# Optimization experiments

Hardware: AMD Instinct MI355X
Metric: run time of the kernel (lower is better)

The kernel has to match this reference:

```python
import jax, jax.numpy as jnp
import numpy as np

N_SENT, B, S, D = 256, 512, 128, 1024
L, LATENT = 10331, 101  # int(sqrt(10331)) == 101


def setup_inputs() -> dict:
    key = jax.random.key(0)
    ks = jax.random.split(key, 16)
    inv = 1.0 / np.sqrt(D)
    return {
        'elmo_outputs': jax.random.normal(ks[0], (N_SENT, S, D), jnp.float32),
        'men_mask': jax.random.randint(ks[1], (B, S), 0, 2).astype(jnp.float32),
        'ctx_mask': jax.random.randint(ks[2], (B, S), 0, 2).astype(jnp.float32),
        'dist': jax.random.uniform(ks[3], (B, S), jnp.float32),
        'gathers': jax.random.randint(ks[4], (B,), 0, N_SENT),
        # nn.Linear weights, stored [out, in] as in torch
        'W_men_m': jax.random.normal(ks[5], (D, D), jnp.float32) * inv,
        'W_men_o': jax.random.normal(ks[6], (1, D), jnp.float32) * inv,
        'W_ctx_c': jax.random.normal(ks[7], (D, D), jnp.float32) * inv,
        'W_ctx_m': jax.random.normal(ks[8], (D, D), jnp.float32) * inv,
        'w_ctx_d': jax.random.normal(ks[9], (D,), jnp.float32),  # Linear(1, D) weight [D,1] squeezed
        'W_ctx_o': jax.random.normal(ks[10], (1, D), jnp.float32) * inv,
        'W_out': jax.random.normal(ks[11], (L, 2 * D), jnp.float32) * (1.0 / np.sqrt(2 * D)),
        'W_f2l': jax.random.normal(ks[12], (LATENT, 2 * D), jnp.float32) * (1.0 / np.sqrt(2 * D)),
        'W_l2l': jax.random.normal(ks[13], (L, LATENT), jnp.float32) * (1.0 / np.sqrt(LATENT)),
        'latent_scalar': jnp.array(0.1, jnp.float32),
    }


def reference(elmo_outputs, men_mask, ctx_mask, dist, gathers,
              W_men_m, W_men_o, W_ctx_c, W_ctx_m, w_ctx_d, W_ctx_o,
              W_out, W_f2l, W_l2l, latent_scalar):
    NEG = -10000.0
    # gather: sentence reps -> mention rows, [B, S, D]
    x = elmo_outputs[gathers]
    # mention additive attention
    men_h = jnp.tanh(jnp.einsum('bsd,ed->bse', x, W_men_m))
    men_score = jnp.einsum('bse,oe->bso', men_h, W_men_o)  # [B,S,1]
    men_score = men_score + (1.0 - men_mask[:, :, None]) * NEG
    men_attn = jax.nn.softmax(men_score, axis=1)
    men_repr = jnp.sum(x * men_attn, axis=1)  # [B, D]
    # context additive attention (dropout layers are identity in eval)
    ctx_h = jnp.tanh(
        jnp.einsum('bsd,ed->bse', x, W_ctx_c)
        + jnp.einsum('bd,ed->be', men_repr, W_ctx_m)[:, None, :]
        + dist[:, :, None] * w_ctx_d
    )
    ctx_score = jnp.einsum('bse,oe->bso', ctx_h, W_ctx_o)
    ctx_score = ctx_score + (1.0 - ctx_mask[:, :, None]) * NEG
    ctx_attn = jax.nn.softmax(ctx_score, axis=1)
    ctx_repr = jnp.sum(x * ctx_attn, axis=1)  # [B, D]
    final_repr = jnp.concatenate([men_repr, ctx_repr], axis=1)  # [B, 2D]
    outputs = final_repr @ W_out.T  # [B, L]
    latent_label = final_repr @ W_f2l.T  # [B, latent]
    outputs_latent = latent_label @ W_l2l.T  # [B, L]
    outputs = outputs + latent_scalar * outputs_latent
    return outputs, outputs_latent
```

## Files before the change

### kernel.cpp

```cpp
#include <hip/hip_runtime.h>
#include <hip/hip_bf16.h>

typedef __bf16 bf16x8 __attribute__((ext_vector_type(8)));
typedef float f32x4 __attribute__((ext_vector_type(4)));
typedef unsigned short u16x8 __attribute__((ext_vector_type(8)));

#define DEV __device__ __forceinline__

static constexpr int N_SENTC = 256, BB = 512, SS = 128, DD = 1024;
static constexpr int LL = 10331, LATENT = 101;
static constexpr int LPAD = 10368;
static constexpr int LATPAD = 128;

DEV float bf2f(unsigned short u) {
  unsigned v = (unsigned)u << 16;
  return __builtin_bit_cast(float, v);
}
DEV unsigned short f2bf(float f) {
  unsigned u = __builtin_bit_cast(unsigned, f);
  unsigned lsb = (u >> 16) & 1u;
  u += 0x7fffu + lsb;
  return (unsigned short)(u >> 16);
}

DEV float fast_tanh(float x) {
  float e = __expf(2.0f * x);
  return 1.0f - 2.0f / (e + 1.0f);
}

DEV void stage8(unsigned short* dst, const float* src) {
  float4 a = *(const float4*)src;
  float4 b = *(const float4*)(src + 4);
  unsigned short t[8];
  t[0] = f2bf(a.x); t[1] = f2bf(a.y); t[2] = f2bf(a.z); t[3] = f2bf(a.w);
  t[4] = f2bf(b.x); t[5] = f2bf(b.y); t[6] = f2bf(b.z); t[7] = f2bf(b.w);
  *(uint4*)dst = *(uint4*)t;
}

DEV void gl_lds16(const unsigned short* g, unsigned short* l) {
  __builtin_amdgcn_global_load_lds(
      (const __attribute__((address_space(1))) unsigned int*)g,
      (__attribute__((address_space(3))) unsigned int*)l, 16, 0, 0);
}

__global__ __launch_bounds__(256) void k_cvt(
    const float* __restrict__ src, unsigned short* __restrict__ dst, int n4) {
  for (int i = blockIdx.x * 256 + threadIdx.x; i < n4; i += gridDim.x * 256) {
    float4 v = ((const float4*)src)[i];
    unsigned short t[4] = {f2bf(v.x), f2bf(v.y), f2bf(v.z), f2bf(v.w)};
    ((uint2*)dst)[i] = *(const uint2*)t;
  }
}

__global__ __launch_bounds__(256) void k_cvt_pad(
    const float* __restrict__ src, unsigned short* __restrict__ dst,
    int srcR, int srcC, int dstC, int total) {
  for (int i = blockIdx.x * 256 + threadIdx.x; i < total; i += gridDim.x * 256) {
    int r = i / dstC, c = i - r * dstC;
    dst[i] = (r < srcR && c < srcC) ? f2bf(src[(size_t)r * srcC + c]) : (unsigned short)0;
  }
}

__global__ __launch_bounds__(512) void k_mc_gemm8(
    const unsigned short* __restrict__ Xb, const unsigned short* __restrict__ Wmb,
    const unsigned short* __restrict__ Wcb, const float* __restrict__ wo,
    float* __restrict__ score, unsigned short* __restrict__ Hc) {
  __shared__ __align__(16) unsigned short lds[2][2][2][8192];
  const int p = blockIdx.x;
  const int tid = threadIdx.x, w = tid >> 6, lane = tid & 63;
  const int lm = lane & 15, lq = lane >> 4;
  const int wr = w >> 2, wc = w & 3;
  const int stRow = w * 16 + (lane >> 2);
  const int stCol = ((lane & 3) * 8) ^ ((lane >> 5) << 4);
  const int rdCol = (lq * 16) ^ ((lane & 8) ? 32 : 0);
  const int aoff = (wr * 16 + lm) * 64 + rdCol;
  const int boff = (wc * 16 + lm) * 64 + rdCol;

  const unsigned short* aSrc;
  const unsigned short* bSrc;
  int rowBase, bcolBase;
  bool isMen;
  auto setTile = [&](int t) {
    const int vbid = p + 256 * t;
    const int lbid = (vbid & 7) * 128 + (vbid >> 3);
    const int colTile = lbid & 7, rowTile = lbid >> 3;
    rowBase = rowTile * 256;
    isMen = colTile < 4;
    bcolBase = (colTile & 3) * 256;
    aSrc = Xb + (size_t)(rowBase + stRow) * 1024 + stCol;
    bSrc = (isMen ? Wmb : Wcb) + (size_t)(bcolBase + stRow) * 1024 + stCol;
  };

  auto ST = [&](int op, int h, int kt, int buf) {
    const unsigned short* s = (op ? bSrc : aSrc) + (size_t)h * 131072 + kt * 64;
    unsigned short* d = &lds[buf][op][h][w * 512];
    gl_lds16(s, d);
    gl_lds16(s + 32, d + 4096);
  };
  auto PRO = [&]() {
    ST(0, 0, 0, 0); ST(1, 0, 0, 0); ST(0, 1, 0, 0); ST(1, 1, 0, 0);
    ST(0, 0, 1, 1); ST(1, 0, 1, 1); ST(0, 1, 1, 1);
  };

  setTile(0);
  PRO();

  for (int t = 0; t < 4; ++t) {
    asm volatile("s_waitcnt vmcnt(6)" ::: "memory");
    __builtin_amdgcn_s_barrier();

    f32x4 acc[8][4] = {};
    bf16x8 af0[4][2], af1[4][2], bfr[4][2];
    for (int kt = 0; kt < 16; ++kt) {
      const int buf = kt & 1;
      const char* A0 = (const char*)&lds[buf][0][0][0];
      const char* A1 = (const char*)&lds[buf][0][1][0];
      const char* B0 = (const char*)&lds[buf][1][0][0];
      const char* B1 = (const char*)&lds[buf][1][1][0];
#pragma unroll
      for (int m = 0; m < 4; ++m)
#pragma unroll
        for (int ks = 0; ks < 2; ++ks)
          af0[m][ks] = *(const bf16x8*)(A0 + aoff + m * 2048 + ks * 8192);
#pragma unroll
      for (int n = 0; n < 2; ++n)
#pragma unroll
        for (int ks = 0; ks < 2; ++ks)
          bfr[n][ks] = *(const bf16x8*)(B0 + boff + n * 4096 + ks * 8192);
      if (kt + 1 < 16) ST(1, 1, kt + 1, buf ^ 1);
      __builtin_amdgcn_s_barrier();
      __builtin_amdgcn_s_setprio(1);
#pragma unroll
      for (int m = 0; m < 4; ++m)
#pragma unroll
        for (int n = 0; n < 2; ++n)
#pragma unroll
          for (int ks = 0; ks < 2; ++ks)
            acc[m][n] = __builtin_amdgcn_mfma_f32_16x16x32_bf16(af0[m][ks], bfr[n][ks], acc[m][n], 0, 0, 0);
      __builtin_amdgcn_s_setprio(0);
      __builtin_amdgcn_s_barrier();
#pragma unroll
      for (int n = 0; n < 2; ++n)
#pragma unroll
        for (int ks = 0; ks < 2; ++ks)
          bfr[2 + n][ks] = *(const bf16x8*)(B1 + boff + n * 4096 + ks * 8192);
      if (kt + 2 < 16) ST(0, 0, kt + 2, buf);
      __builtin_amdgcn_s_barrier();
      __builtin_amdgcn_s_setprio(1);
#pragma unroll
      for (int m = 0; m < 4; ++m)
#pragma unroll
        for (int n = 0; n < 2; ++n)
#pragma unroll
          for (int ks = 0; ks < 2; ++ks)
            acc[m][2 + n] = __builtin_amdgcn_mfma_f32_16x16x32_bf16(af0[m][ks], bfr[2 + n][ks], acc[m][2 + n], 0, 0, 0);
      __builtin_amdgcn_s_setprio(0);
      __builtin_amdgcn_s_barrier();
#pragma unroll
      for (int m = 0; m < 4; ++m)
#pragma unroll
        for (int ks = 0; ks < 2; ++ks)
          af1[m][ks] = *(const bf16x8*)(A1 + aoff + m * 2048 + ks * 8192);
      if (kt + 2 < 16) ST(1, 0, kt + 2, buf);
      __builtin_amdgcn_s_barrier();
      __builtin_amdgcn_s_setprio(1);
#pragma unroll
      for (int m = 0; m < 4; ++m)
#pragma unroll
        for (int n = 0; n < 2; ++n)
#pragma unroll
          for (int ks = 0; ks < 2; ++ks)
            acc[4 + m][n] = __builtin_amdgcn_mfma_f32_16x16x32_bf16(af1[m][ks], bfr[n][ks], acc[4 + m][n], 0, 0, 0);
      __builtin_amdgcn_s_setprio(0);
      __builtin_amdgcn_s_barrier();
      if (kt + 2 < 16) ST(0, 1, kt + 2, buf);
      __builtin_amdgcn_s_barrier();
      __builtin_amdgcn_s_setprio(1);
#pragma unroll
      for (int m = 0; m < 4; ++m)
#pragma unroll
        for (int n = 0; n < 2; ++n)
#pragma unroll
          for (int ks = 0; ks < 2; ++ks)
            acc[4 + m][2 + n] = __builtin_amdgcn_mfma_f32_16x16x32_bf16(af1[m][ks], bfr[2 + n][ks], acc[4 + m][2 + n], 0, 0, 0);
      __builtin_amdgcn_s_setprio(0);
      if (kt < 14) {
        asm volatile("s_waitcnt vmcnt(6)" ::: "memory");
      } else {
        asm volatile("s_waitcnt vmcnt(0)" ::: "memory");
      }
      __builtin_amdgcn_s_barrier();
    }

    if (isMen) {
      float wov[4];
#pragma unroll
      for (int n = 0; n < 4; ++n) wov[n] = wo[bcolBase + n * 64 + wc * 16 + lm];
      float rsum[8][4];
#pragma unroll
      for (int m = 0; m < 8; ++m)
#pragma unroll
        for (int r = 0; r < 4; ++r) {
          float s = 0.f;
#pragma unroll
          for (int n = 0; n < 4; ++n) s += fast_tanh(acc[m][n][r]) * wov[n];
          rsum[m][r] = s;
        }
#pragma unroll
      for (int msk = 1; msk <= 8; msk <<= 1)
#pragma unroll
        for (int m = 0; m < 8; ++m)
#pragma unroll
          for (int r = 0; r < 4; ++r) rsum[m][r] += __shfl_xor(rsum[m][r], msk, 64);
      if (lm == 0) {
#pragma unroll
        for (int m = 0; m < 8; ++m)
#pragma unroll
          for (int r = 0; r < 4; ++r)
            atomicAdd(&score[rowBase + m * 32 + wr * 16 + lq * 4 + r], rsum[m][r]);
      }
    } else {
      const int cb0 = bcolBase + wc * 16 + lm;
#pragma unroll
      for (int m = 0; m < 8; ++m) {
        const int row = rowBase + m * 32 + wr * 16 + lq * 4;
#pragma unroll
        for (int n = 0; n < 4; ++n) {
          const int col = cb0 + n * 64;
#pragma unroll
          for (int r = 0; r < 4; ++r)
            Hc[(size_t)(row + r) * 1024 + col] = f2bf(acc[m][n][r]);
        }
      }
    }
    if (t < 3) {
      setTile(t + 1);
      PRO();
    }
  }
}

__global__ __launch_bounds__(256) void k_ctx_score(
    const unsigned short* __restrict__ Hc, const int* __restrict__ gathers,
    const float* __restrict__ cb, const float* __restrict__ wd,
    const float* __restrict__ wo, const float* __restrict__ dist,
    float* __restrict__ score) {
  const int b = blockIdx.x, tid = threadIdx.x, wave = tid >> 6, lane = tid & 63;
  const int n = gathers[b];
  __shared__ float cbl[1024], wdl[1024], wol[1024];
  for (int i = tid; i < 1024; i += 256) {
    cbl[i] = cb[b * 1024 + i];
    wdl[i] = wd[i];
    wol[i] = wo[i];
  }
  __syncthreads();
  for (int s = wave; s < 128; s += 4) {
    float d = dist[b * 128 + s];
    const unsigned short* hrow = &Hc[(size_t)(n * 128 + s) * 1024 + lane * 16];
    unsigned short hs[16];
    *(uint4*)hs = *(const uint4*)hrow;
    *(uint4*)(hs + 8) = *(const uint4*)(hrow + 8);
    float p = 0.f;
#pragma unroll
    for (int j = 0; j < 16; ++j) {
      int e = lane * 16 + j;
      p += fast_tanh(bf2f(hs[j]) + cbl[e] + d * wdl[e]) * wol[e];
    }
#pragma unroll
    for (int msk = 1; msk <= 32; msk <<= 1) p += __shfl_xor(p, msk, 64);
    if (lane == 0) score[b * 128 + s] = p;
  }
}

__global__ __launch_bounds__(256) void k_softb(
    const float* __restrict__ score_src, const float* __restrict__ mask,
    const unsigned short* __restrict__ Xb, const int* __restrict__ gathers,
    unsigned short* __restrict__ finalrb, int isCtx) {
  const int b = blockIdx.x, tid = threadIdx.x;
  const int n = gathers[b];
  __shared__ float attn[128];
  __shared__ float red[128 * 8];
  __shared__ float smax, ssum;
  if (tid < 128) {
    int srow = isCtx ? b : n;
    attn[tid] = score_src[srow * 128 + tid] + (1.0f - mask[b * 128 + tid]) * (-10000.0f);
  }
  __syncthreads();
  if (tid < 64) {
    float m = fmaxf(attn[tid], attn[tid + 64]);
#pragma unroll
    for (int msk = 1; msk <= 32; msk <<= 1) m = fmaxf(m, __shfl_xor(m, msk, 64));
    if (tid == 0) smax = m;
  }
  __syncthreads();
  if (tid < 128) attn[tid] = __expf(attn[tid] - smax);
  __syncthreads();
  if (tid < 64) {
    float s = attn[tid] + attn[tid + 64];
#pragma unroll
    for (int msk = 1; msk <= 32; msk <<= 1) s += __shfl_xor(s, msk, 64);
    if (tid == 0) ssum = 1.0f / s;
  }
  __syncthreads();
  if (tid < 128) attn[tid] *= ssum;
  __syncthreads();
  const unsigned short* xb = Xb + (size_t)n * 128 * 1024;
  const int c = tid & 127, h = tid >> 7;
  float acc[8] = {};
  for (int s = h; s < 128; s += 2) {
    float w = attn[s];
    u16x8 v = *(const u16x8*)&xb[(size_t)s * 1024 + c * 8];
#pragma unroll
    for (int j = 0; j < 8; ++j) acc[j] += w * bf2f(v[j]);
  }
  if (h == 1) {
#pragma unroll
    for (int j = 0; j < 8; ++j) red[c * 8 + j] = acc[j];
  }
  __syncthreads();
  if (h == 0) {
    unsigned short o[8];
#pragma unroll
    for (int j = 0; j < 8; ++j) o[j] = f2bf(acc[j] + red[c * 8 + j]);
    *(uint4*)&finalrb[(size_t)b * 2048 + (isCtx ? 1024 : 0) + c * 8] = *(uint4*)o;
  }
}

__global__ __launch_bounds__(256) void k_cb_gemm_b(
    const unsigned short* __restrict__ finalrb, const unsigned short* __restrict__ Wcmb,
    float* __restrict__ cb) {
  __shared__ __align__(16) unsigned short As[64 * 32];
  __shared__ __align__(16) unsigned short Bs[64 * 32];
  const int bid = blockIdx.x;
  const int rowBase = (bid >> 4) * 64, colBase = (bid & 15) * 64;
  const int tid = threadIdx.x, wave = tid >> 6, lane = tid & 63;
  const int lm = lane & 15, lq = lane >> 4;
  const int sr = tid >> 2, sc = (tid & 3) * 8;
  f32x4 acc[4] = {};
  for (int k0 = 0; k0 < 1024; k0 += 32) {
    __syncthreads();
    *(uint4*)&As[sr * 32 + sc] = *(const uint4*)&finalrb[(size_t)(rowBase + sr) * 2048 + k0 + sc];
    *(uint4*)&Bs[sr * 32 + sc] = *(const uint4*)&Wcmb[(size_t)(colBase + sr) * 1024 + k0 + sc];
    __syncthreads();
    bf16x8 af = *(const bf16x8*)&As[(wave * 16 + lm) * 32 + lq * 8];
#pragma unroll
    for (int j = 0; j < 4; ++j) {
      bf16x8 bfr = *(const bf16x8*)&Bs[(j * 16 + lm) * 32 + lq * 8];
      acc[j] = __builtin_amdgcn_mfma_f32_16x16x32_bf16(af, bfr, acc[j], 0, 0, 0);
    }
  }
#pragma unroll
  for (int j = 0; j < 4; ++j) {
    int col = colBase + j * 16 + lm;
#pragma unroll
    for (int r = 0; r < 4; ++r) {
      int row = rowBase + wave * 16 + lq * 4 + r;
      cb[row * 1024 + col] = acc[j][r];
    }
  }
}

__global__ __launch_bounds__(256) void k_lat_split(
    const unsigned short* __restrict__ finalrb, const unsigned short* __restrict__ Wf2lb,
    float* __restrict__ latf) {
  __shared__ __align__(16) unsigned short As[64 * 32];
  __shared__ __align__(16) unsigned short Bs[64 * 32];
  const int bid = blockIdx.x;
  const int ks = bid & 7;
  const int rowBase = ((bid >> 3) & 7) * 64;
  const int colBase = (bid >> 6) * 64;
  const int tid = threadIdx.x, wave = tid >> 6, lane = tid & 63;
  const int lm = lane & 15, lq = lane >> 4;
  const int sr = tid >> 2, sc = (tid & 3) * 8;
  f32x4 acc[4] = {};
  const int kEnd = ks * 256 + 256;
  for (int k0 = ks * 256; k0 < kEnd; k0 += 32) {
    __syncthreads();
    *(uint4*)&As[sr * 32 + sc] = *(const uint4*)&finalrb[(size_t)(rowBase + sr) * 2048 + k0 + sc];
    *(uint4*)&Bs[sr * 32 + sc] = *(const uint4*)&Wf2lb[(size_t)(colBase + sr) * 2048 + k0 + sc];
    __syncthreads();
    bf16x8 af = *(const bf16x8*)&As[(wave * 16 + lm) * 32 + lq * 8];
#pragma unroll
    for (int j = 0; j < 4; ++j) {
      bf16x8 bfr = *(const bf16x8*)&Bs[(j * 16 + lm) * 32 + lq * 8];
      acc[j] = __builtin_amdgcn_mfma_f32_16x16x32_bf16(af, bfr, acc[j], 0, 0, 0);
    }
  }
#pragma unroll
  for (int j = 0; j < 4; ++j) {
    int col = colBase + j * 16 + lm;
#pragma unroll
    for (int r = 0; r < 4; ++r) {
      int row = rowBase + wave * 16 + lq * 4 + r;
      atomicAdd(&latf[row * LATPAD + col], acc[j][r]);
    }
  }
}

__global__ __launch_bounds__(256) void k_out_gemm_f(
    const unsigned short* __restrict__ finalrb, const float* __restrict__ Wout,
    const unsigned short* __restrict__ latb, const unsigned short* __restrict__ Wl2lb,
    const float* __restrict__ lscale, float* __restrict__ out,
    float* __restrict__ outLat) {
  __shared__ __align__(16) unsigned short As[2 * 128 * 32];
  __shared__ __align__(16) unsigned short Bs[2 * 128 * 32];
  const int bid = blockIdx.x;
  const int xcd = bid & 7, idx = bid >> 3;
  const int rowTile = idx & 3, colTile = xcd + 8 * (idx >> 2);
  if (colTile >= 81) return;
  const int colBase = colTile * 128;
  const int rowBase = rowTile * 128;
  const int tid = threadIdx.x, wave = tid >> 6, lane = tid & 63;
  const int lm = lane & 15, lq = lane >> 4;
  const int wr = (wave & 1) * 64, wc = (wave >> 1) * 64;
  const int srow = wave * 32 + (lane >> 2);
  const int scol = (lane & 3) * 8;
  const float scal = lscale[0];
  const unsigned short* aPtr = finalrb + (size_t)(rowBase + srow) * 2048 + scol;
  const int br = tid >> 1, bh = tid & 1;
  const int bRow = colBase + br;
  const bool bv = bRow < LL;
  const float* bsrc = Wout + (size_t)bRow * 2048 + bh * 32;
  unsigned short* bdst = &Bs[bh * 4096 + br * 32];
  f32x4 acc[4][4] = {};
  for (int k0 = 0; k0 < 2048; k0 += 64) {
    __syncthreads();
    gl_lds16(aPtr + k0, As + wave * 1024);
    gl_lds16(aPtr + k0 + 16 * 2048, As + wave * 1024 + 512);
    gl_lds16(aPtr + k0 + 32, As + 4096 + wave * 1024);
    gl_lds16(aPtr + k0 + 32 + 16 * 2048, As + 4096 + wave * 1024 + 512);
    if (bv) {
      stage8(bdst, bsrc + k0);
      stage8(bdst + 8, bsrc + k0 + 8);
      stage8(bdst + 16, bsrc + k0 + 16);
      stage8(bdst + 24, bsrc + k0 + 24);
    } else {
      uint4 z = {0, 0, 0, 0};
      *(uint4*)bdst = z;
      *(uint4*)(bdst + 8) = z;
      *(uint4*)(bdst + 16) = z;
      *(uint4*)(bdst + 24) = z;
    }
    __syncthreads();
#pragma unroll
    for (int h = 0; h < 2; ++h) {
      bf16x8 af[4], bfr[4];
#pragma unroll
      for (int m = 0; m < 4; ++m)
        af[m] = *(const bf16x8*)&As[h * 4096 + (wr + m * 16 + lm) * 32 + lq * 8];
#pragma unroll
      for (int n = 0; n < 4; ++n)
        bfr[n] = *(const bf16x8*)&Bs[h * 4096 + (wc + n * 16 + lm) * 32 + lq * 8];
#pragma unroll
      for (int m = 0; m < 4; ++m)
#pragma unroll
        for (int n = 0; n < 4; ++n)
          acc[m][n] = __builtin_amdgcn_mfma_f32_16x16x32_bf16(af[m], bfr[n], acc[m][n], 0, 0, 0);
    }
  }
  const unsigned short* aPtr2 = latb + (size_t)(rowBase + srow) * LATPAD + scol;
  const unsigned short* bPtr2 = Wl2lb + (size_t)(colBase + srow) * LATPAD + scol;
  f32x4 acc2[4][4] = {};
  for (int k0 = 0; k0 < 128; k0 += 64) {
    __syncthreads();
#pragma unroll
    for (int h = 0; h < 2; ++h) {
      gl_lds16(aPtr2 + k0 + h * 32, As + h * 4096 + wave * 1024);
      gl_lds16(aPtr2 + k0 + h * 32 + 16 * LATPAD, As + h * 4096 + wave * 1024 + 512);
      gl_lds16(bPtr2 + k0 + h * 32, Bs + h * 4096 + wave * 1024);
      gl_lds16(bPtr2 + k0 + h * 32 + 16 * LATPAD, Bs + h * 4096 + wave * 1024 + 512);
    }
    __syncthreads();
#pragma unroll
    for (int h = 0; h < 2; ++h) {
      bf16x8 af[4], bfr[4];
#pragma unroll
      for (int m = 0; m < 4; ++m)
        af[m] = *(const bf16x8*)&As[h * 4096 + (wr + m * 16 + lm) * 32 + lq * 8];
#pragma unroll
      for (int n = 0; n < 4; ++n)
        bfr[n] = *(const bf16x8*)&Bs[h * 4096 + (wc + n * 16 + lm) * 32 + lq * 8];
#pragma unroll
      for (int m = 0; m < 4; ++m)
#pragma unroll
        for (int n = 0; n < 4; ++n)
          acc2[m][n] = __builtin_amdgcn_mfma_f32_16x16x32_bf16(af[m], bfr[n], acc2[m][n], 0, 0, 0);
    }
  }
#pragma unroll
  for (int m = 0; m < 4; ++m)
#pragma unroll
    for (int n = 0; n < 4; ++n) {
      int col = colBase + wc + n * 16 + lm;
      if (col < LL) {
#pragma unroll
        for (int r = 0; r < 4; ++r) {
          int row = rowBase + wr + m * 16 + lq * 4 + r;
          float lv = acc2[m][n][r];
          out[(size_t)row * LL + col] = acc[m][n][r] + scal * lv;
          outLat[(size_t)row * LL + col] = lv;
        }
      }
    }
}

__global__ __launch_bounds__(256) void k_men_gemm(
    const float* __restrict__ X, const float* __restrict__ Wm,
    const float* __restrict__ wo, float* __restrict__ score) {
  __shared__ __align__(16) unsigned short As[64 * 32];
  __shared__ __align__(16) unsigned short Bs[64 * 32];
  const int bid = blockIdx.x;
  const int rowBase = (bid >> 4) * 64, colBase = (bid & 15) * 64;
  const int tid = threadIdx.x, wave = tid >> 6, lane = tid & 63;
  const int lm = lane & 15, lq = lane >> 4;
  const int sr = tid >> 2, sc = (tid & 3) * 8;
  f32x4 acc[4] = {};
  for (int k0 = 0; k0 < 1024; k0 += 32) {
    __syncthreads();
    stage8(&As[sr * 32 + sc], &X[(size_t)(rowBase + sr) * 1024 + k0 + sc]);
    stage8(&Bs[sr * 32 + sc], &Wm[(size_t)(colBase + sr) * 1024 + k0 + sc]);
    __syncthreads();
    bf16x8 af = *(const bf16x8*)&As[(wave * 16 + lm) * 32 + lq * 8];
#pragma unroll
    for (int j = 0; j < 4; ++j) {
      bf16x8 bfr = *(const bf16x8*)&Bs[(j * 16 + lm) * 32 + lq * 8];
      acc[j] = __builtin_amdgcn_mfma_f32_16x16x32_bf16(af, bfr, acc[j], 0, 0, 0);
    }
  }
  float rsum[4] = {0.f, 0.f, 0.f, 0.f};
#pragma unroll
  for (int j = 0; j < 4; ++j) {
    float w = wo[colBase + j * 16 + lm];
#pragma unroll
    for (int r = 0; r < 4; ++r) rsum[r] += tanhf(acc[j][r]) * w;
  }
#pragma unroll
  for (int m = 1; m <= 8; m <<= 1)
#pragma unroll
    for (int r = 0; r < 4; ++r) rsum[r] += __shfl_xor(rsum[r], m, 64);
  if (lm == 0) {
    int row0 = rowBase + wave * 16 + lq * 4;
#pragma unroll
    for (int r = 0; r < 4; ++r) atomicAdd(&score[row0 + r], rsum[r]);
  }
}

__global__ __launch_bounds__(256) void k_ctx_gemm(
    const float* __restrict__ X, const int* __restrict__ gathers,
    const float* __restrict__ Wc, const float* __restrict__ wd,
    const float* __restrict__ wo, const float* __restrict__ dist,
    const float* __restrict__ cb, float* __restrict__ score) {
  __shared__ __align__(16) unsigned short As[64 * 32];
  __shared__ __align__(16) unsigned short Bs[64 * 32];
  const int bid = blockIdx.x;
  const int rowBase = (bid >> 4) * 64, colBase = (bid & 15) * 64;
  const int tid = threadIdx.x, wave = tid >> 6, lane = tid & 63;
  const int lm = lane & 15, lq = lane >> 4;
  const int sr = tid >> 2, sc = (tid & 3) * 8;
  const int row_g = rowBase + sr;
  const int srcRow = (gathers[row_g >> 7] << 7) + (row_g & 127);
  f32x4 acc[4] = {};
  for (int k0 = 0; k0 < 1024; k0 += 32) {
    __syncthreads();
    stage8(&As[sr * 32 + sc], &X[(size_t)srcRow * 1024 + k0 + sc]);
    stage8(&Bs[sr * 32 + sc], &Wc[(size_t)(colBase + sr) * 1024 + k0 + sc]);
    __syncthreads();
    bf16x8 af = *(const bf16x8*)&As[(wave * 16 + lm) * 32 + lq * 8];
#pragma unroll
    for (int j = 0; j < 4; ++j) {
      bf16x8 bfr = *(const bf16x8*)&Bs[(j * 16 + lm) * 32 + lq * 8];
      acc[j] = __builtin_amdgcn_mfma_f32_16x16x32_bf16(af, bfr, acc[j], 0, 0, 0);
    }
  }
  float rsum[4] = {0.f, 0.f, 0.f, 0.f};
#pragma unroll
  for (int j = 0; j < 4; ++j) {
    int col = colBase + j * 16 + lm;
    float w = wo[col];
    float wdv = wd[col];
#pragma unroll
    for (int r = 0; r < 4; ++r) {
      int rg = rowBase + wave * 16 + lq * 4 + r;
      int b = rg >> 7, s = rg & 127;
      float v = acc[j][r] + cb[b * 1024 + col] + dist[b * 128 + s] * wdv;
      rsum[r] += tanhf(v) * w;
    }
  }
#pragma unroll
  for (int m = 1; m <= 8; m <<= 1)
#pragma unroll
    for (int r = 0; r < 4; ++r) rsum[r] += __shfl_xor(rsum[r], m, 64);
  if (lm == 0) {
    int row0 = rowBase + wave * 16 + lq * 4;
#pragma unroll
    for (int r = 0; r < 4; ++r) atomicAdd(&score[row0 + r], rsum[r]);
  }
}

__global__ __launch_bounds__(256) void k_soft(
    const float* __restrict__ score_src, const float* __restrict__ mask,
    const float* __restrict__ X, const int* __restrict__ gathers,
    float* __restrict__ finalr, int isCtx) {
  const int b = blockIdx.x, tid = threadIdx.x;
  const int n = gathers[b];
  __shared__ float attn[128];
  __shared__ float smax, ssum;
  if (tid < 128) {
    int srow = isCtx ? b : n;
    attn[tid] = score_src[srow * 128 + tid] + (1.0f - mask[b * 128 + tid]) * (-10000.0f);
  }
  __syncthreads();
  if (tid == 0) {
    float m = attn[0];
    for (int i = 1; i < 128; ++i) m = fmaxf(m, attn[i]);
    smax = m;
  }
  __syncthreads();
  if (tid < 128) attn[tid] = expf(attn[tid] - smax);
  __syncthreads();
  if (tid == 0) {
    float s = 0.f;
    for (int i = 0; i < 128; ++i) s += attn[i];
    ssum = 1.0f / s;
  }
  __syncthreads();
  if (tid < 128) attn[tid] *= ssum;
  __syncthreads();
  const float* xb = &X[(size_t)(n << 7) * 1024];
  const int off = isCtx ? 1024 : 0;
  for (int d = tid; d < 1024; d += 256) {
    float a = 0.f;
#pragma unroll 8
    for (int s = 0; s < 128; ++s) a += attn[s] * xb[s * 1024 + d];
    finalr[b * 2048 + off + d] = a;
  }
}

__global__ __launch_bounds__(256) void k_cb_gemm(
    const float* __restrict__ finalr, const float* __restrict__ Wcm,
    float* __restrict__ cb) {
  __shared__ __align__(16) unsigned short As[64 * 32];
  __shared__ __align__(16) unsigned short Bs[64 * 32];
  const int bid = blockIdx.x;
  const int rowBase = (bid >> 4) * 64, colBase = (bid & 15) * 64;
  const int tid = threadIdx.x, wave = tid >> 6, lane = tid & 63;
  const int lm = lane & 15, lq = lane >> 4;
  const int sr = tid >> 2, sc = (tid & 3) * 8;
  f32x4 acc[4] = {};
  for (int k0 = 0; k0 < 1024; k0 += 32) {
    __syncthreads();
    stage8(&As[sr * 32 + sc], &finalr[(size_t)(rowBase + sr) * 2048 + k0 + sc]);
    stage8(&Bs[sr * 32 + sc], &Wcm[(size_t)(colBase + sr) * 1024 + k0 + sc]);
    __syncthreads();
    bf16x8 af = *(const bf16x8*)&As[(wave * 16 + lm) * 32 + lq * 8];
#pragma unroll
    for (int j = 0; j < 4; ++j) {
      bf16x8 bfr = *(const bf16x8*)&Bs[(j * 16 + lm) * 32 + lq * 8];
      acc[j] = __builtin_amdgcn_mfma_f32_16x16x32_bf16(af, bfr, acc[j], 0, 0, 0);
    }
  }
#pragma unroll
  for (int j = 0; j < 4; ++j) {
    int col = colBase + j * 16 + lm;
#pragma unroll
    for (int r = 0; r < 4; ++r) {
      int row = rowBase + wave * 16 + lq * 4 + r;
      cb[row * 1024 + col] = acc[j][r];
    }
  }
}

__global__ __launch_bounds__(256) void k_lat_gemm(
    const float* __restrict__ finalr, const float* __restrict__ Wf2l,
    float* __restrict__ lat) {
  __shared__ __align__(16) unsigned short As[64 * 32];
  __shared__ __align__(16) unsigned short Bs[64 * 32];
  const int rowBase = blockIdx.y * 64, colBase = blockIdx.x * 64;
  const int tid = threadIdx.x, wave = tid >> 6, lane = tid & 63;
  const int lm = lane & 15, lq = lane >> 4;
  const int sr = tid >> 2, sc = (tid & 3) * 8;
  f32x4 acc[4] = {};
  for (int k0 = 0; k0 < 2048; k0 += 32) {
    __syncthreads();
    stage8(&As[sr * 32 + sc], &finalr[(size_t)(rowBase + sr) * 2048 + k0 + sc]);
    int l = colBase + sr;
    if (l < LATENT) {
      stage8(&Bs[sr * 32 + sc], &Wf2l[(size_t)l * 2048 + k0 + sc]);
    } else {
      uint4 z = {0, 0, 0, 0};
      *(uint4*)&Bs[sr * 32 + sc] = z;
    }
    __syncthreads();
    bf16x8 af = *(const bf16x8*)&As[(wave * 16 + lm) * 32 + lq * 8];
#pragma unroll
    for (int j = 0; j < 4; ++j) {
      bf16x8 bfr = *(const bf16x8*)&Bs[(j * 16 + lm) * 32 + lq * 8];
      acc[j] = __builtin_amdgcn_mfma_f32_16x16x32_bf16(af, bfr, acc[j], 0, 0, 0);
    }
  }
#pragma unroll
  for (int j = 0; j < 4; ++j) {
    int col = colBase + j * 16 + lm;
    if (col < LATENT) {
#pragma unroll
      for (int r = 0; r < 4; ++r) {
        int row = rowBase + wave * 16 + lq * 4 + r;
        lat[row * LATENT + col] = acc[j][r];
      }
    }
  }
}

__global__ __launch_bounds__(256) void k_out_gemm(
    const float* __restrict__ finalr, const float* __restrict__ Wout,
    const float* __restrict__ lat, const float* __restrict__ Wl2l,
    const float* __restrict__ lscale, float* __restrict__ out,
    float* __restrict__ outLat) {
  __shared__ __align__(16) unsigned short As[64 * 32];
  __shared__ __align__(16) unsigned short Bs[64 * 32];
  const int rowBase = blockIdx.y * 64, colBase = blockIdx.x * 64;
  const int tid = threadIdx.x, wave = tid >> 6, lane = tid & 63;
  const int lm = lane & 15, lq = lane >> 4;
  const int sr = tid >> 2, sc = (tid & 3) * 8;
  const float scal = lscale[0];
  const int lrow = colBase + sr;
  const bool lvalid = (lrow < LL);
  f32x4 acc[4] = {};
  for (int k0 = 0; k0 < 2048; k0 += 32) {
    __syncthreads();
    stage8(&As[sr * 32 + sc], &finalr[(size_t)(rowBase + sr) * 2048 + k0 + sc]);
    if (lvalid) {
      stage8(&Bs[sr * 32 + sc], &Wout[(size_t)lrow * 2048 + k0 + sc]);
    } else {
      uint4 z = {0, 0, 0, 0};
      *(uint4*)&Bs[sr * 32 + sc] = z;
    }
    __syncthreads();
    bf16x8 af = *(const bf16x8*)&As[(wave * 16 + lm) * 32 + lq * 8];
#pragma unroll
    for (int j = 0; j < 4; ++j) {
      bf16x8 bfr = *(const bf16x8*)&Bs[(j * 16 + lm) * 32 + lq * 8];
      acc[j] = __builtin_amdgcn_mfma_f32_16x16x32_bf16(af, bfr, acc[j], 0, 0, 0);
    }
  }
  f32x4 acc2[4] = {};
  for (int k2 = 0; k2 < 128; k2 += 32) {
    __syncthreads();
    const int brow = rowBase + sr;
#pragma unroll
    for (int jj = 0; jj < 8; ++jj) {
      int idx = k2 + sc + jj;
      As[sr * 32 + sc + jj] = (idx < LATENT) ? f2bf(lat[brow * LATENT + idx]) : (unsigned short)0;
      Bs[sr * 32 + sc + jj] = (lvalid && idx < LATENT) ? f2bf(Wl2l[lrow * LATENT + idx]) : (unsigned short)0;
    }
    __syncthreads();
    bf16x8 af = *(const bf16x8*)&As[(wave * 16 + lm) * 32 + lq * 8];
#pragma unroll
    for (int j = 0; j < 4; ++j) {
      bf16x8 bfr = *(const bf16x8*)&Bs[(j * 16 + lm) * 32 + lq * 8];
      acc2[j] = __builtin_amdgcn_mfma_f32_16x16x32_bf16(af, bfr, acc2[j], 0, 0, 0);
    }
  }
#pragma unroll
  for (int j = 0; j < 4; ++j) {
    int col = colBase + j * 16 + lm;
    if (col < LL) {
#pragma unroll
      for (int r = 0; r < 4; ++r) {
        int row = rowBase + wave * 16 + lq * 4 + r;
        float lv = acc2[j][r];
        out[(size_t)row * LL + col] = acc[j][r] + scal * lv;
        outLat[(size_t)row * LL + col] = lv;
      }
    }
  }
}

extern "C" void kernel_launch(void* const* d_in, const int* in_sizes, int n_in,
                              void* d_out, int out_size, void* d_ws, size_t ws_size,
                              hipStream_t stream) {
  const float* X = (const float*)d_in[0];
  const float* men_mask = (const float*)d_in[1];
  const float* ctx_mask = (const float*)d_in[2];
  const float* dist = (const float*)d_in[3];
  const int* gathers = (const int*)d_in[4];
  const float* W_men_m = (const float*)d_in[5];
  const float* W_men_o = (const float*)d_in[6];
  const float* W_ctx_c = (const float*)d_in[7];
  const float* W_ctx_m = (const float*)d_in[8];
  const float* w_ctx_d = (const float*)d_in[9];
  const float* W_ctx_o = (const float*)d_in[10];
  const float* W_out = (const float*)d_in[11];
  const float* W_f2l = (const float*)d_in[12];
  const float* W_l2l = (const float*)d_in[13];
  const float* lscale = (const float*)d_in[14];
  float* out = (float*)d_out;
  float* outLat = out + (size_t)BB * LL;

  size_t off = 0;
  auto carve = [&](size_t bytes) {
    void* p = (char*)d_ws + off;
    off = (off + bytes + 255) & ~(size_t)255;
    return p;
  };
  float* sent_score = (float*)carve(32768 * 4);
  float* ctx_score = (float*)carve(65536 * 4);
  float* finalr = (float*)carve((size_t)512 * 2048 * 4);
  float* cb = (float*)carve((size_t)512 * 1024 * 4);
  float* lat = (float*)carve((size_t)512 * LATENT * 4);
  unsigned short* Xb = (unsigned short*)carve((size_t)32768 * 1024 * 2);
  unsigned short* Wmb = (unsigned short*)carve((size_t)1024 * 1024 * 2);
  unsigned short* Wcb = (unsigned short*)carve((size_t)1024 * 1024 * 2);
  unsigned short* Wcmb = (unsigned short*)carve((size_t)1024 * 1024 * 2);
  unsigned short* Hc = (unsigned short*)carve((size_t)32768 * 1024 * 2);
  unsigned short* Wf2lb = (unsigned short*)carve((size_t)LATPAD * 2048 * 2);
  unsigned short* Wl2lb = (unsigned short*)carve((size_t)LPAD * LATPAD * 2);
  unsigned short* finalrb = (unsigned short*)carve((size_t)512 * 2048 * 2);
  unsigned short* latb = (unsigned short*)carve((size_t)512 * LATPAD * 2);
  float* latf = (float*)carve((size_t)512 * LATPAD * 4);
  const bool fits = off <= ws_size;

  if (fits) {
    hipMemsetAsync(sent_score, 0, 32768 * sizeof(float), stream);
    hipMemsetAsync(latf, 0, (size_t)512 * LATPAD * sizeof(float), stream);
    k_cvt<<<8192, 256, 0, stream>>>(X, Xb, 32768 * 1024 / 4);
    k_cvt<<<1024, 256, 0, stream>>>(W_men_m, Wmb, 1024 * 1024 / 4);
    k_cvt<<<1024, 256, 0, stream>>>(W_ctx_c, Wcb, 1024 * 1024 / 4);
    k_cvt<<<1024, 256, 0, stream>>>(W_ctx_m, Wcmb, 1024 * 1024 / 4);
    k_cvt_pad<<<512, 256, 0, stream>>>(W_f2l, Wf2lb, LATENT, 2048, 2048, LATPAD * 2048);
    k_cvt_pad<<<1024, 256, 0, stream>>>(W_l2l, Wl2lb, LL, LATENT, LATPAD, LPAD * LATPAD);
    k_mc_gemm8<<<256, 512, 0, stream>>>(Xb, Wmb, Wcb, W_men_o, sent_score, Hc);
    k_softb<<<512, 256, 0, stream>>>(sent_score, men_mask, Xb, gathers, finalrb, 0);
    k_cb_gemm_b<<<128, 256, 0, stream>>>(finalrb, Wcmb, cb);
    k_ctx_score<<<512, 256, 0, stream>>>(Hc, gathers, cb, w_ctx_d, W_ctx_o, dist, ctx_score);
    k_softb<<<512, 256, 0, stream>>>(ctx_score, ctx_mask, Xb, gathers, finalrb, 1);
    k_lat_split<<<128, 256, 0, stream>>>(finalrb, Wf2lb, latf);
    k_cvt<<<64, 256, 0, stream>>>(latf, latb, 512 * LATPAD / 4);
    k_out_gemm_f<<<352, 256, 0, stream>>>(finalrb, W_out, latb, Wl2lb,
                                          lscale, out, outLat);
  } else {
    hipMemsetAsync(d_ws, 0, (32768 + 65536) * sizeof(float), stream);
    k_men_gemm<<<8192, 256, 0, stream>>>(X, W_men_m, W_men_o, sent_score);
    k_soft<<<512, 256, 0, stream>>>(sent_score, men_mask, X, gathers, finalr, 0);
    k_cb_gemm<<<128, 256, 0, stream>>>(finalr, W_ctx_m, cb);
    k_ctx_gemm<<<16384, 256, 0, stream>>>(X, gathers, W_ctx_c, w_ctx_d, W_ctx_o, dist, cb, ctx_score);
    k_soft<<<512, 256, 0, stream>>>(ctx_score, ctx_mask, X, gathers, finalr, 1);
    k_lat_gemm<<<dim3(2, 8), 256, 0, stream>>>(finalr, W_f2l, lat);
    k_out_gemm<<<dim3(162, 8), 256, 0, stream>>>(finalr, W_out, lat, W_l2l, lscale, out, outLat);
  }
}
```

Before: 657.4 us.

## Fuse weight conversions, fuse ctx score with softmax, prefetch W_out in out GEMM

Five weight-conversion launches are merged into one k_cvt_all kernel. The context score kernel now also does the masked softmax and the weighted sum over X, so the separate k_softb launch and the score round-trip through global memory go away. The output GEMM register-prefetches the next fp32 W_out slice before the barrier and uses manual waitcnt/s_barrier, so global loads overlap with MFMA work. This reduces launch overhead and hides load latency, at the cost of more registers and hand-managed synchronisation.

```diff
diff --git a/kernel.cpp b/kernel.cpp
--- a/kernel.cpp
+++ b/kernel.cpp
@@ -52,12 +52,47 @@
   }
 }
 
-__global__ __launch_bounds__(256) void k_cvt_pad(
-    const float* __restrict__ src, unsigned short* __restrict__ dst,
-    int srcR, int srcC, int dstC, int total) {
-  for (int i = blockIdx.x * 256 + threadIdx.x; i < total; i += gridDim.x * 256) {
-    int r = i / dstC, c = i - r * dstC;
-    dst[i] = (r < srcR && c < srcC) ? f2bf(src[(size_t)r * srcC + c]) : (unsigned short)0;
+__global__ __launch_bounds__(256) void k_cvt_all(
+    const float* __restrict__ Wm, const float* __restrict__ Wc,
+    const float* __restrict__ Wcm, const float* __restrict__ Wf2l,
+    const float* __restrict__ Wl2l,
+    unsigned short* __restrict__ Wmb, unsigned short* __restrict__ Wcb,
+    unsigned short* __restrict__ Wcmb, unsigned short* __restrict__ Wf2lb,
+    unsigned short* __restrict__ Wl2lb) {
+  const int NA = 3 * 262144;
+  const int NB = 65536;
+  const int NC = 331776;
+  for (int u = blockIdx.x * 256 + threadIdx.x; u < NA + NB + NC; u += gridDim.x * 256) {
+    if (u < NA) {
+      int which = u >> 18, off = u & 262143;
+      const float* s = which == 0 ? Wm : (which == 1 ? Wc : Wcm);
+      unsigned short* d = which == 0 ? Wmb : (which == 1 ? Wcb : Wcmb);
+      float4 v = ((const float4*)s)[off];
+      unsigned short t[4] = {f2bf(v.x), f2bf(v.y), f2bf(v.z), f2bf(v.w)};
+      ((uint2*)d)[off] = *(const uint2*)t;
+    } else if (u < NA + NB) {
+      int off = u - NA;
+      int r = off >> 9;
+      if (r < LATENT) {
+        float4 v = ((const float4*)Wf2l)[off];
+        unsigned short t[4] = {f2bf(v.x), f2bf(v.y), f2bf(v.z), f2bf(v.w)};
+        ((uint2*)Wf2lb)[off] = *(const uint2*)t;
+      } else {
+        ((uint2*)Wf2lb)[off] = make_uint2(0, 0);
+      }
+    } else {
+      int off = u - NA - NB;
+      int idx = off * 4;
+      int r = idx >> 7, c0 = idx & 127;
+      unsigned short t[4];
+#pragma unroll
+      for (int j = 0; j < 4; ++j) {
+        int c = c0 + j;
+        t[j] = (r < LL && c < LATENT) ? f2bf(Wl2l[(size_t)r * LATENT + c])
+                                      : (unsigned short)0;
+      }
+      ((uint2*)Wl2lb)[off] = *(const uint2*)t;
+    }
   }
 }
 
@@ -240,14 +275,18 @@
   }
 }
 
-__global__ __launch_bounds__(256) void k_ctx_score(
+__global__ __launch_bounds__(256) void k_ctx_fused(
     const unsigned short* __restrict__ Hc, const int* __restrict__ gathers,
     const float* __restrict__ cb, const float* __restrict__ wd,
     const float* __restrict__ wo, const float* __restrict__ dist,
-    float* __restrict__ score) {
+    const float* __restrict__ mask, const unsigned short* __restrict__ Xb,
+    unsigned short* __restrict__ finalrb) {
   const int b = blockIdx.x, tid = threadIdx.x, wave = tid >> 6, lane = tid & 63;
   const int n = gathers[b];
   __shared__ float cbl[1024], wdl[1024], wol[1024];
+  __shared__ float attn[128];
+  __shared__ float red[128 * 8];
+  __shared__ float smax, ssum;
   for (int i = tid; i < 1024; i += 256) {
     cbl[i] = cb[b * 1024 + i];
     wdl[i] = wd[i];
@@ -268,7 +307,46 @@
     }
 #pragma unroll
     for (int msk = 1; msk <= 32; msk <<= 1) p += __shfl_xor(p, msk, 64);
-    if (lane == 0) score[b * 128 + s] = p;
+    if (lane == 0) attn[s] = p + (1.0f - mask[b * 128 + s]) * (-10000.0f);
+  }
+  __syncthreads();
+  if (tid < 64) {
+    float m = fmaxf(attn[tid], attn[tid + 64]);
+#pragma unroll
+    for (int msk = 1; msk <= 32; msk <<= 1) m = fmaxf(m, __shfl_xor(m, msk, 64));
+    if (tid == 0) smax = m;
+  }
+  __syncthreads();
+  if (tid < 128) attn[tid] = __expf(attn[tid] - smax);
+  __syncthreads();
+  if (tid < 64) {
+    float s = attn[tid] + attn[tid + 64];
+#pragma unroll
+    for (int msk = 1; msk <= 32; msk <<= 1) s += __shfl_xor(s, msk, 64);
+    if (tid == 0) ssum = 1.0f / s;
+  }
+  __syncthreads();
+  if (tid < 128) attn[tid] *= ssum;
+  __syncthreads();
+  const unsigned short* xb = Xb + (size_t)n * 128 * 1024;
+  const int c = tid & 127, h = tid >> 7;
+  float acc[8] = {};
+  for (int s = h; s < 128; s += 2) {
+    float w = attn[s];
+    u16x8 v = *(const u16x8*)&xb[(size_t)s * 1024 + c * 8];
+#pragma unroll
+    for (int j = 0; j < 8; ++j) acc[j] += w * bf2f(v[j]);
+  }
+  if (h == 1) {
+#pragma unroll
+    for (int j = 0; j < 8; ++j) red[c * 8 + j] = acc[j];
+  }
+  __syncthreads();
+  if (h == 0) {
+    unsigned short o[8];
+#pragma unroll
+    for (int j = 0; j < 8; ++j) o[j] = f2bf(acc[j] + red[c * 8 + j]);
+    *(uint4*)&finalrb[(size_t)b * 2048 + 1024 + c * 8] = *(uint4*)o;
   }
 }
 
@@ -420,28 +498,46 @@
   const int br = tid >> 1, bh = tid & 1;
   const int bRow = colBase + br;
   const bool bv = bRow < LL;
-  const float* bsrc = Wout + (size_t)bRow * 2048 + bh * 32;
+  const float* bsrc = Wout + (size_t)(bv ? bRow : 0) * 2048 + bh * 32;
   unsigned short* bdst = &Bs[bh * 4096 + br * 32];
+  float4 fa[8];
+#pragma unroll
+  for (int j = 0; j < 8; ++j) fa[j] = *(const float4*)(bsrc + j * 4);
   f32x4 acc[4][4] = {};
   for (int k0 = 0; k0 < 2048; k0 += 64) {
-    __syncthreads();
+    __builtin_amdgcn_s_barrier();
     gl_lds16(aPtr + k0, As + wave * 1024);
     gl_lds16(aPtr + k0 + 16 * 2048, As + wave * 1024 + 512);
     gl_lds16(aPtr + k0 + 32, As + 4096 + wave * 1024);
     gl_lds16(aPtr + k0 + 32 + 16 * 2048, As + 4096 + wave * 1024 + 512);
-    if (bv) {
-      stage8(bdst, bsrc + k0);
-      stage8(bdst + 8, bsrc + k0 + 8);
-      stage8(bdst + 16, bsrc + k0 + 16);
-      stage8(bdst + 24, bsrc + k0 + 24);
+    {
+      unsigned short t[32];
+#pragma unroll
+      for (int j = 0; j < 8; ++j) {
+        t[4 * j + 0] = f2bf(fa[j].x); t[4 * j + 1] = f2bf(fa[j].y);
+        t[4 * j + 2] = f2bf(fa[j].z); t[4 * j + 3] = f2bf(fa[j].w);
+      }
+      if (bv) {
+#pragma unroll
+        for (int j = 0; j < 4; ++j) *(uint4*)(bdst + 8 * j) = *(uint4*)(t + 8 * j);
+      } else {
+        uint4 z = {0, 0, 0, 0};
+#pragma unroll
+        for (int j = 0; j < 4; ++j) *(uint4*)(bdst + 8 * j) = z;
+      }
+    }
+    __builtin_amdgcn_sched_barrier(0);
+    if (k0 < 1984) {
+#pragma unroll
+      for (int j = 0; j < 8; ++j) fa[j] = *(const float4*)(bsrc + k0 + 64 + j * 4);
+      asm volatile("s_waitcnt lgkmcnt(0)" ::: "memory");
+      asm volatile("s_waitcnt vmcnt(8)" ::: "memory");
     } else {
-      uint4 z = {0, 0, 0, 0};
-      *(uint4*)bdst = z;
-      *(uint4*)(bdst + 8) = z;
-      *(uint4*)(bdst + 16) = z;
-      *(uint4*)(bdst + 24) = z;
-    }
-    __syncthreads();
+      asm volatile("s_waitcnt lgkmcnt(0)" ::: "memory");
+      asm volatile("s_waitcnt vmcnt(0)" ::: "memory");
+    }
+    __builtin_amdgcn_sched_barrier(0);
+    __builtin_amdgcn_s_barrier();
 #pragma unroll
     for (int h = 0; h < 2; ++h) {
       bf16x8 af[4], bfr[4];
@@ -824,16 +920,13 @@
     hipMemsetAsync(sent_score, 0, 32768 * sizeof(float), stream);
     hipMemsetAsync(latf, 0, (size_t)512 * LATPAD * sizeof(float), stream);
     k_cvt<<<8192, 256, 0, stream>>>(X, Xb, 32768 * 1024 / 4);
-    k_cvt<<<1024, 256, 0, stream>>>(W_men_m, Wmb, 1024 * 1024 / 4);
-    k_cvt<<<1024, 256, 0, stream>>>(W_ctx_c, Wcb, 1024 * 1024 / 4);
-    k_cvt<<<1024, 256, 0, stream>>>(W_ctx_m, Wcmb, 1024 * 1024 / 4);
-    k_cvt_pad<<<512, 256, 0, stream>>>(W_f2l, Wf2lb, LATENT, 2048, 2048, LATPAD * 2048);
-    k_cvt_pad<<<1024, 256, 0, stream>>>(W_l2l, Wl2lb, LL, LATENT, LATPAD, LPAD * LATPAD);
+    k_cvt_all<<<2048, 256, 0, stream>>>(W_men_m, W_ctx_c, W_ctx_m, W_f2l, W_l2l,
+                                        Wmb, Wcb, Wcmb, Wf2lb, Wl2lb);
     k_mc_gemm8<<<256, 512, 0, stream>>>(Xb, Wmb, Wcb, W_men_o, sent_score, Hc);
     k_softb<<<512, 256, 0, stream>>>(sent_score, men_mask, Xb, gathers, finalrb, 0);
     k_cb_gemm_b<<<128, 256, 0, stream>>>(finalrb, Wcmb, cb);
-    k_ctx_score<<<512, 256, 0, stream>>>(Hc, gathers, cb, w_ctx_d, W_ctx_o, dist, ctx_score);
-    k_softb<<<512, 256, 0, stream>>>(ctx_score, ctx_mask, Xb, gathers, finalrb, 1);
+    k_ctx_fused<<<512, 256, 0, stream>>>(Hc, gathers, cb, w_ctx_d, W_ctx_o, dist,
+                                         ctx_mask, Xb, finalrb);
     k_lat_split<<<128, 256, 0, stream>>>(finalrb, Wf2lb, latf);
     k_cvt<<<64, 256, 0, stream>>>(latf, latb, 512 * LATPAD / 4);
     k_out_gemm_f<<<352, 256, 0, stream>>>(finalrb, W_out, latb, Wl2lb,
```

After: 652.4 us. Within noise of the previous version (-0.8%).
